# Kernel optimization log

Hardware: AMD Instinct MI355X
Metric: run time of the kernel (lower is better)

The kernel has to match this reference:

```python
import jax, jax.numpy as jnp
import numpy as np

N, E = 2048, 262144
H, EH, NH, FF = 96, 64, 12, 192
DH = H // NH
NITERS, NLAYERS = 2, 3


def _leaky(x):
    return jax.nn.leaky_relu(x, 0.01)


def _ln(x, s, b):
    m = x.mean(-1, keepdims=True)
    v = ((x - m) ** 2).mean(-1, keepdims=True)
    return (x - m) / jnp.sqrt(v + 1e-5) * s + b


def _encoder(x, qkv_w, qkv_b, out_w, out_b, l1s, l1b, fw1, fb1, fw2, fb2, l2s, l2b):
    qkv = x @ qkv_w + qkv_b  # [N, 3H]
    q, k, v = jnp.split(qkv, 3, axis=-1)
    q = q.reshape(-1, NH, DH)
    k = k.reshape(-1, NH, DH)
    v = v.reshape(-1, NH, DH)
    att = jax.nn.softmax(jnp.einsum('nhd,mhd->hnm', q, k) / jnp.sqrt(jnp.float32(DH)), axis=-1)
    o = jnp.einsum('hnm,mhd->nhd', att, v).reshape(-1, H) @ out_w + out_b
    x = _ln(x + o, l1s, l1b)
    f = jax.nn.relu(x @ fw1 + fb1) @ fw2 + fb2
    return _ln(x + f, l2s, l2b)


def setup_inputs() -> dict:
    key = jax.random.key(0)
    ks = iter(jax.random.split(key, 64))
    def p(shape, scale=0.05):
        return (jax.random.normal(next(ks), shape) * scale).astype(jnp.float32)
    inp = {}
    inp['X'] = jax.random.normal(next(ks), (N, 19), dtype=jnp.float32)
    inp['edge_features'] = jax.random.uniform(next(ks), (E, 12), dtype=jnp.float32)
    inp['edge_index'] = jax.random.randint(next(ks), (E, 2), 0, N, dtype=jnp.int32)
    inp['node_scaler'] = jnp.ones((19,), jnp.float32)
    inp['edge_scaler'] = jnp.ones((12,), jnp.float32)
    inp['in_w1'] = p((19, H)); inp['in_b1'] = p((H,))
    inp['in_w2'] = p((H, H)); inp['in_b2'] = p((H,))
    inp['enc_qkv_w'] = p((NLAYERS, H, 3 * H)); inp['enc_qkv_b'] = p((NLAYERS, 3 * H))
    inp['enc_out_w'] = p((NLAYERS, H, H)); inp['enc_out_b'] = p((NLAYERS, H))
    inp['enc_ln1_s'] = jnp.ones((NLAYERS, H), jnp.float32); inp['enc_ln1_b'] = jnp.zeros((NLAYERS, H), jnp.float32)
    inp['enc_ff_w1'] = p((NLAYERS, H, FF)); inp['enc_ff_b1'] = p((NLAYERS, FF))
    inp['enc_ff_w2'] = p((NLAYERS, FF, H)); inp['enc_ff_b2'] = p((NLAYERS, H))
    inp['enc_ln2_s'] = jnp.ones((NLAYERS, H), jnp.float32); inp['enc_ln2_b'] = jnp.zeros((NLAYERS, H), jnp.float32)
    inp['ein_w1'] = p((12, EH)); inp['ein_b1'] = p((EH,))
    inp['ein_w2'] = p((EH, EH)); inp['ein_b2'] = p((EH,))
    inp['ad_w1'] = p((EH, EH)); inp['ad_b1'] = p((EH,))
    inp['ad_w2'] = p((EH, 1)); inp['ad_b2'] = p((1,))
    inp['ar_w1'] = p((EH, EH)); inp['ar_b1'] = p((EH,))
    inp['ar_w2'] = p((EH, 1)); inp['ar_b2'] = p((1,))
    inp['gc_w1'] = p((NITERS, 2 * H, 2 * H)); inp['gc_b1'] = p((NITERS, 2 * H))
    inp['gc_w2'] = p((NITERS, 2 * H, H)); inp['gc_b2'] = p((NITERS, H))
    inp['en_w1'] = p((2 * H + 12 + EH, H)); inp['en_b1'] = p((H,))
    inp['en_w2'] = p((H, 1)); inp['en_b2'] = p((1,))
    return inp


def reference(X, edge_features, edge_index, node_scaler, edge_scaler,
              in_w1, in_b1, in_w2, in_b2,
              enc_qkv_w, enc_qkv_b, enc_out_w, enc_out_b,
              enc_ln1_s, enc_ln1_b, enc_ff_w1, enc_ff_b1, enc_ff_w2, enc_ff_b2,
              enc_ln2_s, enc_ln2_b,
              ein_w1, ein_b1, ein_w2, ein_b2,
              ad_w1, ad_b1, ad_w2, ad_b2,
              ar_w1, ar_b1, ar_w2, ar_b2,
              gc_w1, gc_b1, gc_w2, gc_b2,
              en_w1, en_b1, en_w2, en_b2):
    ef = (edge_features + 1e-4) / edge_scaler
    x = X / node_scaler
    # edge feature MLP + direct/reverse attention weights
    ef_nn = _leaky(_leaky(ef @ ein_w1 + ein_b1) @ ein_w2 + ein_b2)
    a_dir = jax.nn.sigmoid(_leaky(ef_nn @ ad_w1 + ad_b1) @ ad_w2 + ad_b2)
    a_rev = jax.nn.sigmoid(_leaky(ef_nn @ ar_w1 + ar_b1) @ ar_w2 + ar_b2)
    alpha = jnp.concatenate([a_dir, a_rev], axis=0)  # [2E, 1]
    # node input MLP + transformer encoder over all N nodes
    h = _leaky(_leaky(x @ in_w1 + in_b1) @ in_w2 + in_b2)
    for i in range(NLAYERS):
        h = _encoder(h, enc_qkv_w[i], enc_qkv_b[i], enc_out_w[i], enc_out_b[i],
                     enc_ln1_s[i], enc_ln1_b[i], enc_ff_w1[i], enc_ff_b1[i],
                     enc_ff_w2[i], enc_ff_b2[i], enc_ln2_s[i], enc_ln2_b[i])
    src = edge_index[:, 0]
    dst = edge_index[:, 1]
    zeros_n = jnp.zeros((N,), edge_index.dtype)
    ind1 = jnp.concatenate([zeros_n, src, dst])  # destinations, [N + 2E]
    ind2 = jnp.concatenate([zeros_n, dst, src])  # sources
    alpha_full = jnp.concatenate([jnp.ones((N, 1), h.dtype), alpha], axis=0)
    for i in range(NITERS):
        m = jnp.concatenate([h[ind1], h[ind2]], axis=-1)  # [N+2E, 2H]
        m = _leaky(_leaky(m @ gc_w1[i] + gc_b1[i]) @ gc_w2[i] + gc_b2[i])
        num = jax.ops.segment_sum(alpha_full * m, ind1, num_segments=N)
        den = jax.ops.segment_sum(alpha_full, ind1, num_segments=N)
        h = num / (den + 1e-8)
    e = jnp.concatenate([h[src], h[dst], ef_nn, ef], axis=-1)
    pred = jax.nn.sigmoid(_leaky(e @ en_w1 + en_b1) @ en_w2 + en_b2)
    return pred
```

## Files before the change

kernel.cpp:

```cpp
#include <hip/hip_runtime.h>

#define NN 2048
#define EE 262144

typedef __attribute__((ext_vector_type(8))) short bf16x8;
typedef __attribute__((ext_vector_type(4))) float f32x4;
typedef unsigned int u32;
typedef unsigned short u16;

__device__ __forceinline__ u16 f2bf(float f){
  u32 u = __builtin_bit_cast(u32, f);
  u32 r = u + 0x7FFFu + ((u >> 16) & 1u);
  return (u16)(r >> 16);
}
__device__ __forceinline__ float bf2f(u16 h){
  u32 u = ((u32)h) << 16;
  return __builtin_bit_cast(float, u);
}
__device__ __forceinline__ int swzb(int byte, int row){ return byte ^ ((row & 7) << 4); }
__device__ __forceinline__ float lrelu(float v){ return fmaxf(v, 0.01f * v); }

static const size_t WS_WT    = 0;
static const size_t WS_EFNN  = 772096;
static const size_t WS_ALPHA = WS_EFNN  + 33554432;
static const size_t WS_H     = WS_ALPHA + 2097152;
static const size_t WS_QKV   = WS_H     + 786432;
static const size_t WS_OBUF  = WS_QKV   + 2359296;
static const size_t WS_TMPA  = WS_OBUF  + 786432;
static const size_t WS_TMPB  = WS_TMPA  + 786432;
static const size_t WS_X1    = WS_TMPB  + 1572864;
static const size_t WS_NUM   = WS_X1    + 786432;
static const size_t WS_DEN   = WS_NUM   + 786432;
static const size_t WS_XS    = WS_DEN   + 8192;
static const size_t WS_HBF   = WS_XS    + 155648;
static const size_t WS_SIDX  = WS_HBF   + 393216;
static const size_t WS_ALPS  = WS_SIDX  + 4194304;
static const size_t WS_CNT   = WS_ALPS  + 2097152;
static const size_t WS_OFFS  = WS_CNT   + 8192;
static const size_t WS_PK    = WS_OFFS  + 8192;

#define IN1T 0
#define IN2T 3072
#define QKVT 12288
#define OUTT 95232
#define FF1T 122880
#define FF2T 178176
#define EIN1T 233472
#define EIN2T 235520
#define AD1T 239616
#define AR1T 243712
#define GC1T 247808
#define GC2T 321536
#define ENAT 358400
#define ENBT 367616
#define ENCT 376832
#define POOL_TOT 386048

#define PK_EIN1 0
#define PK_EIN2 2048
#define PK_AD1  6144
#define PK_AR1  10240
#define PK_GC2  14336
#define PK_ENC  51200
#define PK_QKV  60416
#define PK_OUT  143360
#define PK_FF1  171008
#define PK_FF2  226304
#define PK_IN1  281600
#define PK_IN2  284672
#define PK_GC1  293888
#define PK_ENAB 367616
#define PK_TOT  386048

struct CvtJobs {
  const float* src[27];
  int K[27], Nc[27], Kp[27];
  int cum[28];
};

__global__ __launch_bounds__(256) void k_cvt(CvtJobs jb, u16* __restrict__ pool){
  int i = blockIdx.x * 256 + threadIdx.x;
  if (i >= jb.cum[27]) return;
  int j = 0;
  while (i >= jb.cum[j + 1]) j++;
  int loc = i - jb.cum[j];
  int Kp = jb.Kp[j];
  int n = loc / Kp, k = loc - n * Kp;
  float v = (k < jb.K[j]) ? jb.src[j][(size_t)k * jb.Nc[j] + n] : 0.f;
  pool[i] = f2bf(v);
}

struct PkJobs {
  int srcOff[27], Nc16[27], Kp[27];
  int cum[28];
};

__global__ __launch_bounds__(256) void k_pack(PkJobs jb, const u16* __restrict__ pool,
                                              u16* __restrict__ pk){
  int i = blockIdx.x * 256 + threadIdx.x;
  if (i >= jb.cum[27]) return;
  int j = 0;
  while (i >= jb.cum[j + 1]) j++;
  int loc = i - jb.cum[j];
  int jj = loc & 7, lane = (loc >> 3) & 63, tk = loc >> 9;
  int Nc16 = jb.Nc16[j];
  int ks = tk / Nc16, t16 = tk - ks * Nc16;
  pk[i] = pool[jb.srcOff[j] + (t16*16 + (lane & 15)) * jb.Kp[j] + ks*32 + (lane >> 4)*8 + jj];
}

__global__ __launch_bounds__(256) void k_xscale(const float* __restrict__ X, const float* __restrict__ ns,
                                                float* __restrict__ xs){
  int i = blockIdx.x * 256 + threadIdx.x;
  if (i < NN * 19) xs[i] = X[i] / ns[i % 19];
}

__global__ __launch_bounds__(256) void k_hist(const int* __restrict__ ei, int* __restrict__ cnt){
  int g = blockIdx.x * 256 + threadIdx.x;
  int i1 = (g < EE) ? ei[2*g] : ei[2*(g - EE) + 1];
  atomicAdd(cnt + i1, 1);
}

__global__ __launch_bounds__(256) void k_scan(const int* __restrict__ cnt, int* __restrict__ offs){
  __shared__ int wsum[4], wbase[4];
  int t = threadIdx.x;
  int base = t * 8;
  int c[8]; int T = 0;
  #pragma unroll
  for (int i = 0; i < 8; i++){ c[i] = cnt[base + i]; T += c[i]; }
  int lane = t & 63, wv = t >> 6;
  int inc = T;
  #pragma unroll
  for (int st = 1; st < 64; st <<= 1){
    int v = __shfl_up(inc, st);
    if (lane >= st) inc += v;
  }
  if (lane == 63) wsum[wv] = inc;
  __syncthreads();
  if (t == 0){ int r = 0; for (int w2 = 0; w2 < 4; w2++){ wbase[w2] = r; r += wsum[w2]; } }
  __syncthreads();
  int run = wbase[wv] + inc - T;
  #pragma unroll
  for (int i = 0; i < 8; i++){ offs[base + i] = run; run += c[i]; }
  if (t == 255) offs[2048] = run;
}

__global__ __launch_bounds__(256) void k_scatter(const int* __restrict__ ei, const float* __restrict__ alpha,
    const int* __restrict__ offs, int* __restrict__ rk, int2* __restrict__ sidx, float* __restrict__ alphaS){
  int g = blockIdx.x * 256 + threadIdx.x;
  int i1, i2;
  if (g < EE){ i1 = ei[2*g]; i2 = ei[2*g + 1]; }
  else { int gg = g - EE; i1 = ei[2*gg + 1]; i2 = ei[2*gg]; }
  int r = atomicAdd(rk + i1, 1);
  int pos = offs[i1] + r;
  sidx[pos] = make_int2(i1, i2);
  alphaS[pos] = alpha[g];
}

__global__ __launch_bounds__(256) void k_dens(const int* __restrict__ offs, const float* __restrict__ alphaS,
                                              float* __restrict__ den){
  int n = blockIdx.x * 4 + (threadIdx.x >> 6);
  int lane = threadIdx.x & 63;
  int b = offs[n], e = offs[n + 1];
  float s = 0.f;
  for (int i = b + lane; i < e; i += 64) s += alphaS[i];
  #pragma unroll
  for (int st = 1; st < 64; st <<= 1) s += __shfl_xor(s, st);
  if (lane == 0) den[n] = s + (n == 0 ? 2048.f : 0.f);
}

template<int NT, int KS, int SR, int NC16>
__device__ __forceinline__ void tile_gemm_gp(const char* sm, int aBase, const u16* __restrict__ Wp,
                                             int lane, f32x4* acc){
  const int r15 = lane & 15;
  const int kb = (lane >> 4) * 16;
  #pragma unroll
  for (int ks = 0; ks < KS; ks++){
    bf16x8 a = *(const bf16x8*)(sm + aBase + swzb(r15*SR + ks*64 + kb, r15));
    #pragma unroll
    for (int ct = 0; ct < NT; ct++){
      bf16x8 b = *(const bf16x8*)(Wp + (((size_t)ks*NC16 + ct)*64 + lane)*8);
      acc[ct] = __builtin_amdgcn_mfma_f32_16x16x32_bf16(a, b, acc[ct], 0, 0, 0);
    }
  }
}

template<int NT, int KS, int MODE, int ACT, int DIVA = 0>
__global__ __launch_bounds__(256) void k_gemm2(const float* __restrict__ A, int K, int NcTot, int Nc16Tot,
    const u16* __restrict__ pkW, const float* __restrict__ bias, float* __restrict__ C,
    float* __restrict__ C2, const float* __restrict__ R, const float* __restrict__ sc,
    const float* __restrict__ bi, const float* __restrict__ dden)
{
  constexpr int Kpad = KS * 32;
  constexpr int SR = (Kpad*2 + 127) / 128 * 128;
  __shared__ __align__(16) char smem[32*SR + 256];
  const int tid = threadIdx.x;
  const int row0 = blockIdx.x * 32;
  for (int j = tid; j < 32*(Kpad/2); j += 256){
    int r = j / (Kpad/2); int c = (j - r*(Kpad/2)) * 2;
    const float* ap = A + (size_t)(row0 + r)*K + c;
    float f0 = (c < K) ? ap[0] : 0.f;
    float f1 = (c + 1 < K) ? ap[1] : 0.f;
    if (DIVA){
      float dv = 1.f / (dden[row0 + r] + 1e-8f);
      f0 *= dv; f1 *= dv;
    }
    *(u32*)(smem + swzb(r*SR + c*2, r)) = (u32)f2bf(f0) | ((u32)f2bf(f1) << 16);
  }
  __syncthreads();
  const int lane = tid & 63, w = tid >> 6;
  const int wr = w >> 1, wc = w & 1;
  const int r15 = lane & 15;
  const int kb = (lane >> 4) * 16;
  f32x4 acc[NT] = {};
  #pragma unroll
  for (int ks = 0; ks < KS; ks++){
    int row = wr*16 + r15;
    bf16x8 a = *(const bf16x8*)(smem + swzb(row*SR + ks*64 + kb, row));
    #pragma unroll
    for (int ct = 0; ct < NT; ct++){
      int t16g = blockIdx.y*(2*NT) + wc*NT + ct;
      bf16x8 b = *(const bf16x8*)(pkW + (((size_t)ks*Nc16Tot + t16g)*64 + lane)*8);
      acc[ct] = __builtin_amdgcn_mfma_f32_16x16x32_bf16(a, b, acc[ct], 0, 0, 0);
    }
  }
  const int colbase = blockIdx.y*(NT*32) + wc*(NT*16);
  if (MODE != 2){
    #pragma unroll
    for (int ct = 0; ct < NT; ct++){
      int col = colbase + ct*16 + r15;
      float bs = bias ? bias[col] : 0.f;
      #pragma unroll
      for (int q = 0; q < 4; q++){
        int row = row0 + wr*16 + (lane >> 4)*4 + q;
        float v = acc[ct][q] + bs;
        if (ACT == 1) v = lrelu(v);
        if (ACT == 2) v = v > 0.f ? v : 0.f;
        if (MODE == 0){
          C[(size_t)row*NcTot + col] = v;
        } else {
          if (col < 96){
            C[(size_t)row*288 + col] = v;
          } else if (col < 192){
            int hh = (col - 96) >> 3, cc = (col - 96) & 7;
            C2[(((size_t)hh*2048 + row) << 4) + cc] = v;
          } else {
            int hh = (col - 192) >> 3, cc = (col - 192) & 7;
            C2[(((size_t)hh*2048 + row) << 4) + 8 + cc] = v;
          }
        }
      }
    }
  } else {
    float* lnb = (float*)(smem + 32*SR);
    float vv[NT][4];
    float ps[4] = {0,0,0,0}, pq[4] = {0,0,0,0};
    #pragma unroll
    for (int ct = 0; ct < NT; ct++){
      int col = colbase + ct*16 + r15;
      float bs = bias[col];
      #pragma unroll
      for (int q = 0; q < 4; q++){
        int row = row0 + wr*16 + (lane >> 4)*4 + q;
        float v = acc[ct][q] + bs + R[(size_t)row*96 + col];
        vv[ct][q] = v;
        ps[q] += v;
        pq[q] += v*v;
      }
    }
    #pragma unroll
    for (int m = 1; m < 16; m <<= 1){
      #pragma unroll
      for (int q = 0; q < 4; q++){
        ps[q] += __shfl_xor(ps[q], m);
        pq[q] += __shfl_xor(pq[q], m);
      }
    }
    if (r15 == 0){
      #pragma unroll
      for (int q = 0; q < 4; q++){
        int row16 = (lane >> 4)*4 + q;
        lnb[(((wr*2 + wc)*16) + row16)*2]     = ps[q];
        lnb[(((wr*2 + wc)*16) + row16)*2 + 1] = pq[q];
      }
    }
    __syncthreads();
    #pragma unroll
    for (int ct = 0; ct < NT; ct++){
      int col = colbase + ct*16 + r15;
      float scv = sc[col], biv = bi[col];
      #pragma unroll
      for (int q = 0; q < 4; q++){
        int row16 = (lane >> 4)*4 + q;
        float s  = lnb[((wr*2)*16 + row16)*2]     + lnb[((wr*2+1)*16 + row16)*2];
        float ss = lnb[((wr*2)*16 + row16)*2 + 1] + lnb[((wr*2+1)*16 + row16)*2 + 1];
        float mean = s * (1.f/96.f);
        float var  = ss * (1.f/96.f) - mean*mean;
        float rs = rsqrtf(var + 1e-5f);
        int row = row0 + wr*16 + row16;
        C[(size_t)row*96 + col] = (vv[ct][q] - mean)*rs*scv + biv;
      }
    }
  }
}

__global__ __launch_bounds__(256) void k_attn5(const float* __restrict__ qkv, const float* __restrict__ kvp,
                                               float* __restrict__ obuf){
  __shared__ float kbuf[2][4096];
  __shared__ float part[4][16][12];
  const int tid = threadIdx.x;
  const int lane = tid & 63, w = tid >> 6;
  const int r = lane & 15, q = lane >> 4;
  const int head = blockIdx.x >> 7, rb = blockIdx.x & 127;
  const int row = rb*16 + r;
  const float* qp = qkv + (size_t)row*288 + head*8;
  float4 qa = *(const float4*)qp;
  float4 qb = *(const float4*)(qp + 4);
  const float* base = kvp + (size_t)head*32768;
  float4 st0 = *(const float4*)(base + tid*4);
  float4 st1 = *(const float4*)(base + 1024 + tid*4);
  float4 st2 = *(const float4*)(base + 2048 + tid*4);
  float4 st3 = *(const float4*)(base + 3072 + tid*4);
  *(float4*)&kbuf[0][tid*4]        = st0;
  *(float4*)&kbuf[0][1024 + tid*4] = st1;
  *(float4*)&kbuf[0][2048 + tid*4] = st2;
  *(float4*)&kbuf[0][3072 + tid*4] = st3;
  __syncthreads();
  float sm = 0.f;
  float o0=0,o1=0,o2=0,o3=0,o4=0,o5=0,o6=0,o7=0;
  for (int c = 0; c < 8; c++){
    if (c < 7){
      const float* nb = base + (c+1)*4096;
      st0 = *(const float4*)(nb + tid*4);
      st1 = *(const float4*)(nb + 1024 + tid*4);
      st2 = *(const float4*)(nb + 2048 + tid*4);
      st3 = *(const float4*)(nb + 3072 + tid*4);
    }
    const float* kp0 = &kbuf[c & 1][(w*64 + q)*16];
    #pragma unroll
    for (int i = 0; i < 16; i++){
      const float* kp = kp0 + i*64;
      float4 ka = *(const float4*)kp;
      float4 kb4 = *(const float4*)(kp + 4);
      float4 va = *(const float4*)(kp + 8);
      float4 vb = *(const float4*)(kp + 12);
      float s = qa.x*ka.x + qa.y*ka.y + qa.z*ka.z + qa.w*ka.w
              + qb.x*kb4.x + qb.y*kb4.y + qb.z*kb4.z + qb.w*kb4.w;
      s = fminf(s * 0.35355339059327373f, 60.f);
      float p = __expf(s);
      sm += p;
      o0 += p*va.x; o1 += p*va.y; o2 += p*va.z; o3 += p*va.w;
      o4 += p*vb.x; o5 += p*vb.y; o6 += p*vb.z; o7 += p*vb.w;
    }
    if (c < 7){
      float* wb = kbuf[(c+1) & 1];
      *(float4*)&wb[tid*4]        = st0;
      *(float4*)&wb[1024 + tid*4] = st1;
      *(float4*)&wb[2048 + tid*4] = st2;
      *(float4*)&wb[3072 + tid*4] = st3;
      __syncthreads();
    }
  }
  #pragma unroll
  for (int stx = 16; stx < 64; stx <<= 1){
    o0 += __shfl_xor(o0, stx); o1 += __shfl_xor(o1, stx);
    o2 += __shfl_xor(o2, stx); o3 += __shfl_xor(o3, stx);
    o4 += __shfl_xor(o4, stx); o5 += __shfl_xor(o5, stx);
    o6 += __shfl_xor(o6, stx); o7 += __shfl_xor(o7, stx);
    sm += __shfl_xor(sm, stx);
  }
  if (q == 0){
    float* pp = part[w][r];
    pp[0]=o0; pp[1]=o1; pp[2]=o2; pp[3]=o3; pp[4]=o4; pp[5]=o5; pp[6]=o6; pp[7]=o7; pp[8]=sm;
  }
  __syncthreads();
  if (tid < 128){
    int rr = tid >> 3, d = tid & 7;
    float o  = part[0][rr][d] + part[1][rr][d] + part[2][rr][d] + part[3][rr][d];
    float ss = part[0][rr][8] + part[1][rr][8] + part[2][rr][8] + part[3][rr][8];
    obuf[(size_t)(rb*16 + rr)*96 + head*8 + d] = o / ss;
  }
}

__global__ __launch_bounds__(256) void k_edge(const float* __restrict__ efr, const float* __restrict__ es,
    const u16* __restrict__ pk,
    const float* __restrict__ eb1, const float* __restrict__ eb2,
    const float* __restrict__ adb1, const float* __restrict__ adw2, const float* __restrict__ adb2,
    const float* __restrict__ arb1, const float* __restrict__ arw2, const float* __restrict__ arb2,
    u16* __restrict__ efnn, float* __restrict__ alpha)
{
  __shared__ __align__(16) char smem[16384];
  const int tid = threadIdx.x;
  const int e0 = blockIdx.x * 64;
  for (int j = tid; j < 64*16; j += 256){
    int r = j >> 4; int c = (j & 15) * 2;
    float f0 = 0.f, f1 = 0.f;
    if (c < 12)     f0 = (efr[(e0+r)*12 + c]     + 1e-4f) / es[c];
    if (c + 1 < 12) f1 = (efr[(e0+r)*12 + c + 1] + 1e-4f) / es[c+1];
    *(u32*)(smem + swzb(r*128 + c*2, r)) = (u32)f2bf(f0) | ((u32)f2bf(f1) << 16);
  }
  __syncthreads();
  const int lane = tid & 63, w = tid >> 6;
  const int r15 = lane & 15;

  auto store_lds = [&](f32x4* acc, int base, const float* bias){
    #pragma unroll
    for (int ct = 0; ct < 4; ct++){
      int col = ct*16 + r15;
      float bs = bias[col];
      #pragma unroll
      for (int q = 0; q < 4; q++){
        int row = w*16 + (lane >> 4)*4 + q;
        *(u16*)(smem + base + swzb(row*128 + col*2, row)) = f2bf(lrelu(acc[ct][q] + bs));
      }
    }
  };

  { f32x4 acc[4] = {};
    tile_gemm_gp<4,1,128,4>(smem, w*2048, pk + PK_EIN1, lane, acc);
    store_lds(acc, 8192, eb1); }
  __syncthreads();
  { f32x4 acc[4] = {};
    tile_gemm_gp<4,2,128,4>(smem, 8192 + w*2048, pk + PK_EIN2, lane, acc);
    store_lds(acc, 0, eb2); }
  __syncthreads();
  for (int j = tid; j < 2048; j += 256){
    int r = j >> 5;
    ((u32*)efnn)[e0*32 + j] = *(const u32*)(smem + swzb(r*128 + (j&31)*4, r));
  }
  { f32x4 acc[4] = {};
    tile_gemm_gp<4,2,128,4>(smem, w*2048, pk + PK_AD1, lane, acc);
    store_lds(acc, 8192, adb1); }
  __syncthreads();
  { int row = tid >> 2, part = tid & 3;
    float s = 0.f;
    #pragma unroll
    for (int i = 0; i < 16; i++){
      int k = part*16 + i;
      s += bf2f(*(const u16*)(smem + 8192 + swzb(row*128 + k*2, row))) * adw2[k];
    }
    s += __shfl_xor(s, 1); s += __shfl_xor(s, 2);
    if (part == 0) alpha[e0 + row] = 1.f / (1.f + __expf(-(s + adb2[0]))); }
  __syncthreads();
  { f32x4 acc[4] = {};
    tile_gemm_gp<4,2,128,4>(smem, w*2048, pk + PK_AR1, lane, acc);
    store_lds(acc, 8192, arb1); }
  __syncthreads();
  { int row = tid >> 2, part = tid & 3;
    float s = 0.f;
    #pragma unroll
    for (int i = 0; i < 16; i++){
      int k = part*16 + i;
      s += bf2f(*(const u16*)(smem + 8192 + swzb(row*128 + k*2, row))) * arw2[k];
    }
    s += __shfl_xor(s, 1); s += __shfl_xor(s, 2);
    if (part == 0) alpha[EE + e0 + row] = 1.f / (1.f + __expf(-(s + arb2[0]))); }
}

__global__ __launch_bounds__(256) void k_gc8(const float* __restrict__ P,
    const int2* __restrict__ sidx, const float* __restrict__ alphaS, const int* __restrict__ offs,
    const u16* __restrict__ wt2p, const float* __restrict__ b1, const float* __restrict__ b2,
    float* __restrict__ num)
{
  __shared__ __align__(16) char smem[26624];
  float* p1c  = (float*)(smem + 24576);
  int*   i2b  = (int*)  (smem + 25344);
  float* alph = (float*)(smem + 25600);
  float* part = (float*)(smem + 25856);
  const int tid = threadIdx.x;
  const int lane = tid & 63, w = tid >> 6;
  const int wr = w >> 1, wc = w & 1;
  const int r15 = lane & 15;
  const int kb = (lane >> 4) * 16;
  const int n = blockIdx.x >> 1, sp = blockIdx.x & 1;
  const int rbeg = offs[n], rend = offs[n + 1];
  if (tid < 192) p1c[tid] = P[(size_t)n*384 + tid] + b1[tid];
  float b2r[3];
  #pragma unroll
  for (int ct = 0; ct < 3; ct++) b2r[ct] = b2[wc*48 + ct*16 + r15];
  float cs0 = 0.f, cs1 = 0.f, cs2 = 0.f;

  const int total = rend - rbeg + (n == 0 ? 1 : 0);
  const int nch = (total + 63) >> 6;
  __syncthreads();
  for (int c = sp; c < nch; c += 2){
    int base = rbeg + c*64;
    if (tid < 64){
      int pos = base + tid;
      if (pos < rend){ i2b[tid] = sidx[pos].y; alph[tid] = alphaS[pos]; }
      else if (n == 0 && pos == rend){ i2b[tid] = 0; alph[tid] = 2048.f; }
      else { i2b[tid] = 0; alph[tid] = 0.f; }
    }
    __syncthreads();
    for (int j = tid; j < 1536; j += 256){
      int r = j / 24, q = j - (j/24)*24;
      int c8 = q * 8;
      const float* p2 = P + (size_t)i2b[r]*384 + 192 + c8;
      float4 b0 = *(const float4*)p2, b1v = *(const float4*)(p2 + 4);
      const float* pc = p1c + c8;
      u16 pkv[8];
      pkv[0]=f2bf(lrelu(pc[0]+b0.x)); pkv[1]=f2bf(lrelu(pc[1]+b0.y));
      pkv[2]=f2bf(lrelu(pc[2]+b0.z)); pkv[3]=f2bf(lrelu(pc[3]+b0.w));
      pkv[4]=f2bf(lrelu(pc[4]+b1v.x)); pkv[5]=f2bf(lrelu(pc[5]+b1v.y));
      pkv[6]=f2bf(lrelu(pc[6]+b1v.z)); pkv[7]=f2bf(lrelu(pc[7]+b1v.w));
      *(bf16x8*)(smem + swzb(r*384 + c8*2, r)) = *(bf16x8*)pkv;
    }
    __syncthreads();
    float ar[2][4];
    #pragma unroll
    for (int rt = 0; rt < 2; rt++)
      #pragma unroll
      for (int q = 0; q < 4; q++)
        ar[rt][q] = alph[wr*32 + rt*16 + (lane >> 4)*4 + q];
    f32x4 acc2[2][3] = {};
    #pragma unroll
    for (int ks = 0; ks < 6; ks++){
      bf16x8 a[2];
      #pragma unroll
      for (int rt = 0; rt < 2; rt++){
        int row = wr*32 + rt*16 + r15;
        a[rt] = *(const bf16x8*)(smem + swzb(row*384 + ks*64 + kb, row));
      }
      #pragma unroll
      for (int ct = 0; ct < 3; ct++){
        bf16x8 b = *(const bf16x8*)(wt2p + (((size_t)ks*6 + wc*3 + ct)*64 + lane)*8);
        #pragma unroll
        for (int rt = 0; rt < 2; rt++)
          acc2[rt][ct] = __builtin_amdgcn_mfma_f32_16x16x32_bf16(a[rt], b, acc2[rt][ct], 0, 0, 0);
      }
    }
    #pragma unroll
    for (int rt = 0; rt < 2; rt++){
      #pragma unroll
      for (int q = 0; q < 4; q++){
        float aw = ar[rt][q];
        cs0 += aw * lrelu(acc2[rt][0][q] + b2r[0]);
        cs1 += aw * lrelu(acc2[rt][1][q] + b2r[1]);
        cs2 += aw * lrelu(acc2[rt][2][q] + b2r[2]);
      }
    }
    __syncthreads();
  }
  #pragma unroll
  for (int stx = 16; stx < 64; stx <<= 1){
    cs0 += __shfl_xor(cs0, stx);
    cs1 += __shfl_xor(cs1, stx);
    cs2 += __shfl_xor(cs2, stx);
  }
  if (lane < 16){
    part[(w*3 + 0)*16 + lane] = cs0;
    part[(w*3 + 1)*16 + lane] = cs1;
    part[(w*3 + 2)*16 + lane] = cs2;
  }
  __syncthreads();
  if (tid < 96){
    int wc2 = tid / 48, rem = tid - wc2*48;
    int ct = rem / 16, rr = rem - ct*16;
    float tot = part[(wc2*3 + ct)*16 + rr] + part[((2 + wc2)*3 + ct)*16 + rr];
    atomicAdd(num + (size_t)n*96 + tid, tot);
  }
}

__global__ __launch_bounds__(256) void k_final3(const float* __restrict__ hp,
    const int* __restrict__ ei, const u16* __restrict__ efnn, const float* __restrict__ efr,
    const float* __restrict__ es, const u16* __restrict__ encp, const float* __restrict__ enb1,
    const float* __restrict__ enw2, const float* __restrict__ enb2, float* __restrict__ out)
{
  __shared__ __align__(16) char smem[38400];
  float* etb = (float*)(smem + 12288);
  float* w2s = (float*)(smem + 37120);
  float* b1s = (float*)(smem + 37504);
  int*   eix = (int*)  (smem + 37888);
  const int tid = threadIdx.x;
  const int e0 = blockIdx.x * 64;
  for (int j = tid; j < 768; j += 256){
    int r = j / 12, q = j - (j/12)*12;
    int e = e0 + r;
    bf16x8 v;
    if (q < 8){
      v = *(const bf16x8*)(efnn + (size_t)e*64 + q*8);
    } else if (q < 10){
      u16 pkv[8];
      #pragma unroll
      for (int i = 0; i < 8; i++){
        int cc = (q - 8)*8 + i;
        pkv[i] = (cc < 12) ? f2bf((efr[(size_t)e*12 + cc] + 1e-4f) / es[cc]) : (u16)0;
      }
      v = *(bf16x8*)pkv;
    } else {
      v = bf16x8{0,0,0,0,0,0,0,0};
    }
    *(bf16x8*)(smem + swzb(r*192 + q*16, r)) = v;
  }
  if (tid < 96) w2s[tid] = enw2[tid];
  else if (tid < 192) b1s[tid - 96] = enb1[tid - 96];
  if (tid < 64){ eix[2*tid] = ei[2*(e0+tid)]; eix[2*tid+1] = ei[2*(e0+tid)+1]; }
  __syncthreads();
  const int lane = tid & 63, w = tid >> 6;
  const int r15 = lane & 15;
  f32x4 acc[6] = {};
  tile_gemm_gp<6,3,192,6>(smem, w*16*192, encp, lane, acc);
  #pragma unroll
  for (int ct = 0; ct < 6; ct++){
    int col = ct*16 + r15;
    #pragma unroll
    for (int q = 0; q < 4; q++){
      int row = w*16 + (lane >> 4)*4 + q;
      etb[row*97 + col] = acc[ct][q];
    }
  }
  __syncthreads();
  int r = tid >> 2, part = tid & 3;
  int s1 = eix[2*r], s2 = eix[2*r + 1];
  const float* p1 = hp + (size_t)s1*192 + part*24;
  const float* p2 = hp + (size_t)s2*192 + 96 + part*24;
  const float* et = etb + r*97 + part*24;
  const float* wz = w2s + part*24;
  const float* bz = b1s + part*24;
  float s = 0.f;
  #pragma unroll
  for (int i = 0; i < 24; i++){
    float v = et[i] + p1[i] + p2[i] + bz[i];
    s += lrelu(v) * wz[i];
  }
  s += __shfl_xor(s, 1); s += __shfl_xor(s, 2);
  if (part == 0) out[e0 + r] = 1.f / (1.f + __expf(-(s + enb2[0])));
}

extern "C" void kernel_launch(void* const* d_in, const int* in_sizes, int n_in,
                              void* d_out, int out_size, void* d_ws, size_t ws_size,
                              hipStream_t stream) {
  (void)in_sizes; (void)n_in; (void)out_size; (void)ws_size;
  const float* X      = (const float*)d_in[0];
  const float* EFR    = (const float*)d_in[1];
  const int*   EI     = (const int*)  d_in[2];
  const float* NS     = (const float*)d_in[3];
  const float* ES     = (const float*)d_in[4];
  const float* IN_W1  = (const float*)d_in[5];
  const float* IN_B1  = (const float*)d_in[6];
  const float* IN_W2  = (const float*)d_in[7];
  const float* IN_B2  = (const float*)d_in[8];
  const float* QKV_W  = (const float*)d_in[9];
  const float* QKV_B  = (const float*)d_in[10];
  const float* OUT_W  = (const float*)d_in[11];
  const float* OUT_B  = (const float*)d_in[12];
  const float* LN1S   = (const float*)d_in[13];
  const float* LN1B   = (const float*)d_in[14];
  const float* FFW1   = (const float*)d_in[15];
  const float* FFB1   = (const float*)d_in[16];
  const float* FFW2   = (const float*)d_in[17];
  const float* FFB2   = (const float*)d_in[18];
  const float* LN2S   = (const float*)d_in[19];
  const float* LN2B   = (const float*)d_in[20];
  const float* EIN_W1 = (const float*)d_in[21];
  const float* EIN_B1 = (const float*)d_in[22];
  const float* EIN_W2 = (const float*)d_in[23];
  const float* EIN_B2 = (const float*)d_in[24];
  const float* AD_W1  = (const float*)d_in[25];
  const float* AD_B1  = (const float*)d_in[26];
  const float* AD_W2  = (const float*)d_in[27];
  const float* AD_B2  = (const float*)d_in[28];
  const float* AR_W1  = (const float*)d_in[29];
  const float* AR_B1  = (const float*)d_in[30];
  const float* AR_W2  = (const float*)d_in[31];
  const float* AR_B2  = (const float*)d_in[32];
  const float* GC_W1  = (const float*)d_in[33];
  const float* GC_B1  = (const float*)d_in[34];
  const float* GC_W2  = (const float*)d_in[35];
  const float* GC_B2  = (const float*)d_in[36];
  const float* EN_W1  = (const float*)d_in[37];
  const float* EN_B1  = (const float*)d_in[38];
  const float* EN_W2  = (const float*)d_in[39];
  const float* EN_B2  = (const float*)d_in[40];

  char* ws = (char*)d_ws;
  u16*   pool   = (u16*)  (ws + WS_WT);
  u16*   efnn   = (u16*)  (ws + WS_EFNN);
  float* alpha  = (float*)(ws + WS_ALPHA);
  float* h      = (float*)(ws + WS_H);
  float* qkvb   = (float*)(ws + WS_QKV);
  float* obuf   = (float*)(ws + WS_OBUF);
  float* tmpA   = (float*)(ws + WS_TMPA);
  float* tmpB   = (float*)(ws + WS_TMPB);
  float* x1     = (float*)(ws + WS_X1);
  float* num    = (float*)(ws + WS_NUM);
  float* den    = (float*)(ws + WS_DEN);
  float* xs     = (float*)(ws + WS_XS);
  int2*  sidx   = (int2*) (ws + WS_SIDX);
  float* alphaS = (float*)(ws + WS_ALPS);
  int*   cnt    = (int*)  (ws + WS_CNT);
  int*   offs   = (int*)  (ws + WS_OFFS);
  u16*   pk     = (u16*)  (ws + WS_PK);
  float* P      = (float*)(ws + WS_QKV);
  float* hp     = (float*)(ws + WS_TMPB);
  float* kvp    = (float*)(ws + WS_ALPHA);

  CvtJobs jb;
  int idx = 0, cum = 0;
  auto addjob = [&](const float* s, int K, int Nc, int Kp){
    jb.src[idx] = s; jb.K[idx] = K; jb.Nc[idx] = Nc; jb.Kp[idx] = Kp;
    jb.cum[idx] = cum; cum += Nc * Kp; idx++;
  };
  addjob(IN_W1, 19, 96, 32);
  addjob(IN_W2, 96, 96, 96);
  for (int l = 0; l < 3; l++) addjob(QKV_W + (size_t)l*96*288, 96, 288, 96);
  for (int l = 0; l < 3; l++) addjob(OUT_W + (size_t)l*96*96,  96, 96,  96);
  for (int l = 0; l < 3; l++) addjob(FFW1  + (size_t)l*96*192, 96, 192, 96);
  for (int l = 0; l < 3; l++) addjob(FFW2  + (size_t)l*192*96, 192, 96, 192);
  addjob(EIN_W1, 12, 64, 32);
  addjob(EIN_W2, 64, 64, 64);
  addjob(AD_W1,  64, 64, 64);
  addjob(AR_W1,  64, 64, 64);
  for (int i = 0; i < 2; i++){
    addjob(GC_W1 + (size_t)i*192*192,          96, 192, 96);
    addjob(GC_W1 + (size_t)i*192*192 + 96*192, 96, 192, 96);
  }
  for (int i = 0; i < 2; i++) addjob(GC_W2 + (size_t)i*192*96, 192, 96, 192);
  addjob(EN_W1,            96, 96, 96);
  addjob(EN_W1 + 96*96,    96, 96, 96);
  addjob(EN_W1 + 192*96,   76, 96, 96);
  jb.cum[idx] = cum;

  k_cvt<<<(POOL_TOT + 255)/256, 256, 0, stream>>>(jb, pool);

  PkJobs pj;
  int pidx = 0, pcum = 0;
  auto addpk = [&](int srcOff, int Nc16, int Ks, int Kp){
    pj.srcOff[pidx] = srcOff; pj.Nc16[pidx] = Nc16; pj.Kp[pidx] = Kp;
    pj.cum[pidx] = pcum; pcum += Nc16 * Ks * 512; pidx++;
  };
  addpk(EIN1T, 4, 1, 32);
  addpk(EIN2T, 4, 2, 64);
  addpk(AD1T,  4, 2, 64);
  addpk(AR1T,  4, 2, 64);
  addpk(GC2T,          6, 6, 192);
  addpk(GC2T + 18432,  6, 6, 192);
  addpk(ENCT, 6, 3, 96);
  for (int l = 0; l < 3; l++) addpk(QKVT + l*27648, 18, 3, 96);
  for (int l = 0; l < 3; l++) addpk(OUTT + l*9216,   6, 3, 96);
  for (int l = 0; l < 3; l++) addpk(FF1T + l*18432, 12, 3, 96);
  for (int l = 0; l < 3; l++) addpk(FF2T + l*18432,  6, 6, 192);
  addpk(IN1T, 6, 1, 32);
  addpk(IN2T, 6, 3, 96);
  for (int i = 0; i < 2; i++) addpk(GC1T + i*36864, 24, 3, 96);
  addpk(ENAT, 12, 3, 96);
  for (int z = pidx; z <= 27; z++) pj.cum[z] = pcum;

  k_pack<<<(PK_TOT + 255)/256, 256, 0, stream>>>(pj, pool, pk);

  k_xscale<<<(NN*19 + 255)/256, 256, 0, stream>>>(X, NS, xs);
  k_gemm2<3,1,0,1><<<dim3(64,1), 256, 0, stream>>>(xs, 19, 96, 6, pk + PK_IN1, IN_B1, tmpA,
                                                   nullptr, nullptr, nullptr, nullptr, nullptr);
  k_gemm2<3,3,0,1><<<dim3(64,1), 256, 0, stream>>>(tmpA, 96, 96, 6, pk + PK_IN2, IN_B2, h,
                                                   nullptr, nullptr, nullptr, nullptr, nullptr);

  k_edge<<<EE/64, 256, 0, stream>>>(EFR, ES, pk, EIN_B1, EIN_B2,
                                    AD_B1, AD_W2, AD_B2, AR_B1, AR_W2, AR_B2, efnn, alpha);

  (void)hipMemsetAsync(cnt, 0, NN*4, stream);
  k_hist<<<(2*EE)/256, 256, 0, stream>>>(EI, cnt);
  k_scan<<<1, 256, 0, stream>>>(cnt, offs);
  (void)hipMemsetAsync(cnt, 0, NN*4, stream);
  k_scatter<<<(2*EE)/256, 256, 0, stream>>>(EI, alpha, offs, cnt, sidx, alphaS);
  k_dens<<<NN/4, 256, 0, stream>>>(offs, alphaS, den);

  for (int l = 0; l < 3; l++){
    k_gemm2<3,3,1,0><<<dim3(64,3), 256, 0, stream>>>(h, 96, 288, 18, pk + PK_QKV + l*27648,
                                                     QKV_B + l*288, qkvb, kvp, nullptr, nullptr, nullptr, nullptr);
    k_attn5<<<1536, 256, 0, stream>>>(qkvb, kvp, obuf);
    k_gemm2<3,3,2,0><<<dim3(64,1), 256, 0, stream>>>(obuf, 96, 96, 6, pk + PK_OUT + l*9216,
                                                     OUT_B + l*96, x1, nullptr, h, LN1S + l*96, LN1B + l*96, nullptr);
    k_gemm2<3,3,0,2><<<dim3(64,2), 256, 0, stream>>>(x1, 96, 192, 12, pk + PK_FF1 + l*18432,
                                                     FFB1 + l*192, tmpB, nullptr, nullptr, nullptr, nullptr, nullptr);
    k_gemm2<3,6,2,0><<<dim3(64,1), 256, 0, stream>>>(tmpB, 192, 96, 6, pk + PK_FF2 + l*18432,
                                                     FFB2 + l*96, h, nullptr, x1, LN2S + l*96, LN2B + l*96, nullptr);
  }

  for (int it = 0; it < 2; it++){
    if (it == 0){
      k_gemm2<3,3,0,0><<<dim3(64,3), 256, 0, stream>>>(h, 96, 384, 24, pk + PK_GC1 + it*36864,
                                                       nullptr, P, nullptr, nullptr, nullptr, nullptr, nullptr);
    } else {
      k_gemm2<3,3,0,0,1><<<dim3(64,3), 256, 0, stream>>>(num, 96, 384, 24, pk + PK_GC1 + it*36864,
                                                         nullptr, P, nullptr, nullptr, nullptr, nullptr, den);
    }
    (void)hipMemsetAsync(num, 0, NN*96*4, stream);
    k_gc8<<<2*NN, 256, 0, stream>>>(P, sidx, alphaS, offs,
                                    pk + PK_GC2 + it*18432, GC_B1 + it*192, GC_B2 + it*96, num);
  }

  k_gemm2<3,3,0,0,1><<<dim3(64,2), 256, 0, stream>>>(num, 96, 192, 12, pk + PK_ENAB,
                                                     nullptr, hp, nullptr, nullptr, nullptr, nullptr, den);
  k_final3<<<EE/64, 256, 0, stream>>>(hp, EI, efnn, EFR, ES,
                                      pk + PK_ENC, EN_B1, EN_W2, EN_B2, (float*)d_out);
}
```

Baseline: 597.5 us.

## Use nontemporal loads/stores for streamed edge data and prefetch gc metadata

Converts streaming global loads and stores of edge indices, edge features, alpha, efnn and the sorted index arrays to nontemporal builtins, so single-use data does not pollute the caches. In the graph-conv kernel, the per-chunk neighbour index and alpha fetch is moved into registers one iteration ahead, overlapping it with the MFMA work of the current chunk. The sidx store is packed into one 64-bit nontemporal write. The risk is that nontemporal hints hurt data that is actually reused later, such as efnn and alpha read by subsequent kernels.

```diff
diff --git a/kernel.cpp b/kernel.cpp
--- a/kernel.cpp
+++ b/kernel.cpp
@@ -5,8 +5,10 @@
 
 typedef __attribute__((ext_vector_type(8))) short bf16x8;
 typedef __attribute__((ext_vector_type(4))) float f32x4;
+typedef __attribute__((ext_vector_type(4))) unsigned int u32x4;
 typedef unsigned int u32;
 typedef unsigned short u16;
+typedef long long s64;
 
 __device__ __forceinline__ u16 f2bf(float f){
   u32 u = __builtin_bit_cast(u32, f);
@@ -116,7 +118,8 @@
 
 __global__ __launch_bounds__(256) void k_hist(const int* __restrict__ ei, int* __restrict__ cnt){
   int g = blockIdx.x * 256 + threadIdx.x;
-  int i1 = (g < EE) ? ei[2*g] : ei[2*(g - EE) + 1];
+  int i1 = (g < EE) ? __builtin_nontemporal_load(ei + 2*g)
+                    : __builtin_nontemporal_load(ei + 2*(g - EE) + 1);
   atomicAdd(cnt + i1, 1);
 }
 
@@ -148,12 +151,20 @@
     const int* __restrict__ offs, int* __restrict__ rk, int2* __restrict__ sidx, float* __restrict__ alphaS){
   int g = blockIdx.x * 256 + threadIdx.x;
   int i1, i2;
-  if (g < EE){ i1 = ei[2*g]; i2 = ei[2*g + 1]; }
-  else { int gg = g - EE; i1 = ei[2*gg + 1]; i2 = ei[2*gg]; }
+  if (g < EE){
+    i1 = __builtin_nontemporal_load(ei + 2*g);
+    i2 = __builtin_nontemporal_load(ei + 2*g + 1);
+  } else {
+    int gg = g - EE;
+    i1 = __builtin_nontemporal_load(ei + 2*gg + 1);
+    i2 = __builtin_nontemporal_load(ei + 2*gg);
+  }
+  float al = __builtin_nontemporal_load(alpha + g);
   int r = atomicAdd(rk + i1, 1);
   int pos = offs[i1] + r;
-  sidx[pos] = make_int2(i1, i2);
-  alphaS[pos] = alpha[g];
+  s64 pk2 = ((s64)(u32)i2 << 32) | (u32)i1;
+  __builtin_nontemporal_store(pk2, (s64*)(sidx + pos));
+  __builtin_nontemporal_store(al, alphaS + pos);
 }
 
 __global__ __launch_bounds__(256) void k_dens(const int* __restrict__ offs, const float* __restrict__ alphaS,
@@ -394,8 +405,8 @@
   for (int j = tid; j < 64*16; j += 256){
     int r = j >> 4; int c = (j & 15) * 2;
     float f0 = 0.f, f1 = 0.f;
-    if (c < 12)     f0 = (efr[(e0+r)*12 + c]     + 1e-4f) / es[c];
-    if (c + 1 < 12) f1 = (efr[(e0+r)*12 + c + 1] + 1e-4f) / es[c+1];
+    if (c < 12)     f0 = (__builtin_nontemporal_load(efr + (size_t)(e0+r)*12 + c)     + 1e-4f) / es[c];
+    if (c + 1 < 12) f1 = (__builtin_nontemporal_load(efr + (size_t)(e0+r)*12 + c + 1) + 1e-4f) / es[c+1];
     *(u32*)(smem + swzb(r*128 + c*2, r)) = (u32)f2bf(f0) | ((u32)f2bf(f1) << 16);
   }
   __syncthreads();
@@ -425,7 +436,8 @@
   __syncthreads();
   for (int j = tid; j < 2048; j += 256){
     int r = j >> 5;
-    ((u32*)efnn)[e0*32 + j] = *(const u32*)(smem + swzb(r*128 + (j&31)*4, r));
+    u32 v = *(const u32*)(smem + swzb(r*128 + (j&31)*4, r));
+    __builtin_nontemporal_store(v, (u32*)efnn + e0*32 + j);
   }
   { f32x4 acc[4] = {};
     tile_gemm_gp<4,2,128,4>(smem, w*2048, pk + PK_AD1, lane, acc);
@@ -439,7 +451,7 @@
       s += bf2f(*(const u16*)(smem + 8192 + swzb(row*128 + k*2, row))) * adw2[k];
     }
     s += __shfl_xor(s, 1); s += __shfl_xor(s, 2);
-    if (part == 0) alpha[e0 + row] = 1.f / (1.f + __expf(-(s + adb2[0]))); }
+    if (part == 0) __builtin_nontemporal_store(1.f / (1.f + __expf(-(s + adb2[0]))), alpha + e0 + row); }
   __syncthreads();
   { f32x4 acc[4] = {};
     tile_gemm_gp<4,2,128,4>(smem, w*2048, pk + PK_AR1, lane, acc);
@@ -453,7 +465,7 @@
       s += bf2f(*(const u16*)(smem + 8192 + swzb(row*128 + k*2, row))) * arw2[k];
     }
     s += __shfl_xor(s, 1); s += __shfl_xor(s, 2);
-    if (part == 0) alpha[EE + e0 + row] = 1.f / (1.f + __expf(-(s + arb2[0]))); }
+    if (part == 0) __builtin_nontemporal_store(1.f / (1.f + __expf(-(s + arb2[0]))), alpha + EE + e0 + row); }
 }
 
 __global__ __launch_bounds__(256) void k_gc8(const float* __restrict__ P,
@@ -481,15 +493,23 @@
 
   const int total = rend - rbeg + (n == 0 ? 1 : 0);
   const int nch = (total + 63) >> 6;
+
+  int pm_i2 = 0; float pm_al = 0.f;
+  auto fetch_meta = [&](int c){
+    if (tid < 64){
+      int pos = rbeg + c*64 + tid;
+      if (pos < rend){
+        s64 v = __builtin_nontemporal_load((const s64*)(sidx + pos));
+        pm_i2 = (int)(v >> 32);
+        pm_al = __builtin_nontemporal_load(alphaS + pos);
+      } else if (n == 0 && pos == rend){ pm_i2 = 0; pm_al = 2048.f; }
+      else { pm_i2 = 0; pm_al = 0.f; }
+    }
+  };
+  fetch_meta(sp);
   __syncthreads();
   for (int c = sp; c < nch; c += 2){
-    int base = rbeg + c*64;
-    if (tid < 64){
-      int pos = base + tid;
-      if (pos < rend){ i2b[tid] = sidx[pos].y; alph[tid] = alphaS[pos]; }
-      else if (n == 0 && pos == rend){ i2b[tid] = 0; alph[tid] = 2048.f; }
-      else { i2b[tid] = 0; alph[tid] = 0.f; }
-    }
+    if (tid < 64){ i2b[tid] = pm_i2; alph[tid] = pm_al; }
     __syncthreads();
     for (int j = tid; j < 1536; j += 256){
       int r = j / 24, q = j - (j/24)*24;
@@ -511,6 +531,7 @@
       #pragma unroll
       for (int q = 0; q < 4; q++)
         ar[rt][q] = alph[wr*32 + rt*16 + (lane >> 4)*4 + q];
+    if (c + 2 < nch) fetch_meta(c + 2);
     f32x4 acc2[2][3] = {};
     #pragma unroll
     for (int ks = 0; ks < 6; ks++){
@@ -577,13 +598,14 @@
     int e = e0 + r;
     bf16x8 v;
     if (q < 8){
-      v = *(const bf16x8*)(efnn + (size_t)e*64 + q*8);
+      u32x4 t = __builtin_nontemporal_load((const u32x4*)(efnn + (size_t)e*64 + q*8));
+      v = __builtin_bit_cast(bf16x8, t);
     } else if (q < 10){
       u16 pkv[8];
       #pragma unroll
       for (int i = 0; i < 8; i++){
         int cc = (q - 8)*8 + i;
-        pkv[i] = (cc < 12) ? f2bf((efr[(size_t)e*12 + cc] + 1e-4f) / es[cc]) : (u16)0;
+        pkv[i] = (cc < 12) ? f2bf((__builtin_nontemporal_load(efr + (size_t)e*12 + cc) + 1e-4f) / es[cc]) : (u16)0;
       }
       v = *(bf16x8*)pkv;
     } else {
@@ -593,7 +615,10 @@
   }
   if (tid < 96) w2s[tid] = enw2[tid];
   else if (tid < 192) b1s[tid - 96] = enb1[tid - 96];
-  if (tid < 64){ eix[2*tid] = ei[2*(e0+tid)]; eix[2*tid+1] = ei[2*(e0+tid)+1]; }
+  if (tid < 64){
+    eix[2*tid]     = __builtin_nontemporal_load(ei + 2*(e0+tid));
+    eix[2*tid + 1] = __builtin_nontemporal_load(ei + 2*(e0+tid) + 1);
+  }
   __syncthreads();
   const int lane = tid & 63, w = tid >> 6;
   const int r15 = lane & 15;
```

Result: slower. 626.3 us (+4.8%).
